# Kernel tuning notes

Measured on AMD Instinct MI355X. Metric: run time of the kernel, lower is better.

Reference implementation:

```python
import jax, jax.numpy as jnp
import numpy as np

B = 1024       # batch of triples
E = 50000      # num_entities
R = 500        # num_relations
D = 512        # dimension
P = 16         # parts
C = 8          # num_cores
ALPHA = 2.0    # -> q = alpha/2 = 1.0
Q = ALPHA / 2.0
DP = D // P    # 32


def setup_inputs() -> dict:
    key = jax.random.key(0)
    ks = jax.random.split(key, 10)
    xav_e = (2.0 / (E + D)) ** 0.5
    xav_r = (2.0 / (R + D)) ** 0.5
    return {
        "heads": jax.random.randint(ks[0], (B,), 0, E),
        "relations": jax.random.randint(ks[1], (B,), 0, R),
        "tails": jax.random.randint(ks[2], (B,), 0, E),
        "entity_w": jax.random.normal(ks[3], (E, D), dtype=jnp.float32) * xav_e,
        "relation_w": jax.random.normal(ks[4], (R, D), dtype=jnp.float32) * xav_r,
        "W_cores": jax.random.uniform(ks[5], (C, P, P, P), dtype=jnp.float32,
                                      minval=-0.01, maxval=0.01),
        "attn_w1": jax.random.normal(ks[6], (2 * D, D), dtype=jnp.float32) * (1.0 / (2 * D)) ** 0.5,
        "attn_b1": jnp.zeros((D,), dtype=jnp.float32),
        "attn_w2": jax.random.normal(ks[7], (D, C), dtype=jnp.float32) * (1.0 / D) ** 0.5,
        "attn_b2": jnp.zeros((C,), dtype=jnp.float32),
    }


def _pq_norm(x):
    # ((|x|^p).sum(2) ** q).sum(1), p=2
    return ((x * x).sum(2) ** Q).sum(1)


def _geometric_consistency(W_cores):
    # center of mass of |W| along each axis, per core; vectorized over cores
    coords = jnp.arange(P, dtype=jnp.float32)
    Wa = jnp.abs(W_cores)                      # [C,P,P,P]
    tot = Wa.sum(axis=(1, 2, 3))               # [C]
    cx = (Wa * coords[None, :, None, None]).sum(axis=(1, 2, 3)) / tot
    cy = (Wa * coords[None, None, :, None]).sum(axis=(1, 2, 3)) / tot
    cz = (Wa * coords[None, None, None, :]).sum(axis=(1, 2, 3)) / tot
    centers = jnp.stack([cx, cy, cz], axis=1)  # [C,3]
    d2 = ((centers[:, None, :] - centers[None, :, :]) ** 2).sum(-1)
    dist = jnp.sqrt(d2)
    masked = dist + jnp.eye(C, dtype=dist.dtype) * 1e6
    min_d = masked.min(axis=1)
    return -jnp.mean(jnp.log(min_d + 1e-6))


def reference(heads, relations, tails, entity_w, relation_w, W_cores,
              attn_w1, attn_b1, attn_w2, attn_b2):
    h = entity_w[heads]          # [B,D]
    r = relation_w[relations]    # [B,D]
    t = entity_w[tails]          # [B,D]

    hr = jnp.concatenate([h, r], axis=1)                       # [B,2D]
    hid = jax.nn.relu(hr @ attn_w1 + attn_b1)                  # [B,D]
    attn = jax.nn.softmax(hid @ attn_w2 + attn_b2, axis=1)     # [B,C]

    h3 = h.reshape(-1, DP, P)
    r3 = r.reshape(-1, DP, P)
    t3 = t.reshape(-1, DP, P)

    h_norm = _pq_norm(h3)
    r_norm = _pq_norm(r3)
    t_norm = _pq_norm(t3)

    # attention-weighted effective core per triple (sum over cores is linear,
    # so folding attn into W before the contraction is exactly the same math)
    Weff = jnp.einsum('bc,cpqs->bpqs', attn, W_cores)          # [B,P,P,P]

    # x1[b,i,s] = sum_{p,q} h[b,i,p] r[b,i,q] W[b,p,q,s]
    x1 = jnp.einsum('bip,biq,bpqs->bis', h3, r3, Weff)
    # x2[b,i,p] = sum_{q,s} r[b,i,q] t[b,i,s] W[b,p,q,s]
    x2 = jnp.einsum('biq,bis,bpqs->bip', r3, t3, Weff)
    # x3[b,i,q] = sum_{p,s} h[b,i,p] t[b,i,s] W[b,p,q,s]
    x3 = jnp.einsum('bip,bis,bpqs->biq', h3, t3, Weff)

    whr_norm = _pq_norm(x1)
    wrt_norm = _pq_norm(x2)
    wth_norm = _pq_norm(x3)

    scores = x1.reshape(-1, D) @ entity_w.T                    # [B,E]

    factor1 = jnp.mean(h_norm) + jnp.mean(r_norm) + jnp.mean(t_norm)
    factor2 = jnp.mean(whr_norm) + jnp.mean(wrt_norm) + jnp.mean(wth_norm)
    factor3 = _geometric_consistency(W_cores)
    return (scores, factor1, factor2, factor3, attn)
```

## Files before the change

### kernel.cpp

```cpp
#include <hip/hip_runtime.h>
#include <cstdint>
#include <cstddef>

#define NB 1024
#define NE 50000
#define NE_PAD 50048
#define DCOL 512
#define ATTN_C 8

static const size_t SCORES_OFF = (size_t)NB * NE;
static const size_t F1_OFF = SCORES_OFF + 0;
static const size_t F2_OFF = SCORES_OFF + 1;
static const size_t F3_OFF = SCORES_OFF + 2;
static const size_t ATTN_OFF = SCORES_OFF + 3;

typedef float f32x4 __attribute__((ext_vector_type(4)));
typedef short s16x8 __attribute__((ext_vector_type(8)));

__device__ __forceinline__ unsigned short f2bf(float f) {
  union { float f; uint32_t u; } x; x.f = f;
  uint32_t u = x.u;
  uint32_t r = (u + 0x7fffu + ((u >> 16) & 1u)) >> 16;
  return (unsigned short)r;
}

__device__ __forceinline__ void gload16(const void* g, void* l) {
  __builtin_amdgcn_global_load_lds(
      (const __attribute__((address_space(1))) uint32_t*)g,
      (__attribute__((address_space(3))) uint32_t*)l, 16, 0, 0);
}

__global__ __launch_bounds__(256)
void gather_hr(const int* __restrict__ heads, const int* __restrict__ rels,
               const int* __restrict__ tails, const float* __restrict__ ew,
               const float* __restrict__ rw, unsigned short* __restrict__ hrb,
               float* __restrict__ n1) {
  int b = blockIdx.x, tid = threadIdx.x;
  const float* h = ew + (size_t)heads[b] * DCOL;
  const float* r = rw + (size_t)rels[b] * DCOL;
  const float* t = ew + (size_t)tails[b] * DCOL;
  float acc = 0.f;
  for (int d = tid; d < DCOL; d += 256) {
    float hv = h[d], rv = r[d], tv = t[d];
    hrb[(size_t)b * 1024 + d] = f2bf(hv);
    hrb[(size_t)b * 1024 + DCOL + d] = f2bf(rv);
    acc += hv * hv + rv * rv + tv * tv;
  }
  __shared__ float red[256];
  red[tid] = acc; __syncthreads();
  for (int s = 128; s > 0; s >>= 1) {
    if (tid < s) red[tid] += red[tid + s];
    __syncthreads();
  }
  if (tid == 0) n1[b] = red[0];
}

__global__ __launch_bounds__(256)
void cvt_pad(const float* __restrict__ src, unsigned short* __restrict__ dst,
             int n4valid, int n4tot) {
  int i = blockIdx.x * 256 + threadIdx.x;
  int stride = gridDim.x * 256;
  for (; i < n4tot; i += stride) {
    float x = 0.f, y = 0.f, z = 0.f, w = 0.f;
    if (i < n4valid) {
      float4 v = ((const float4*)src)[i];
      x = v.x; y = v.y; z = v.z; w = v.w;
    }
    union { unsigned short u[4]; uint2 v2; } o;
    o.u[0] = f2bf(x); o.u[1] = f2bf(y); o.u[2] = f2bf(z); o.u[3] = f2bf(w);
    ((uint2*)dst)[i] = o.v2;
  }
}

__global__ __launch_bounds__(256)
void transpose_w1(const float* __restrict__ w1, unsigned short* __restrict__ w1t) {
  __shared__ float tile[32][33];
  int tx = threadIdx.x & 31, ty = threadIdx.x >> 5;
  int kb = blockIdx.y * 32, nb = blockIdx.x * 32;
  #pragma unroll
  for (int rr = 0; rr < 32; rr += 8)
    tile[ty + rr][tx] = w1[(size_t)(kb + ty + rr) * 512 + nb + tx];
  __syncthreads();
  #pragma unroll
  for (int rr = 0; rr < 32; rr += 8)
    w1t[(size_t)(nb + ty + rr) * 1024 + kb + tx] = f2bf(tile[tx][ty + rr]);
}

template <int EPI>
__global__ __launch_bounds__(256, 2)
void gemm_nt(const unsigned short* __restrict__ A, const unsigned short* __restrict__ B,
             float* __restrict__ C, const float* __restrict__ bias,
             int M, int N, int K, int Nc) {
  __shared__ __align__(16) uint8_t smem[32768];
  const int tid = threadIdx.x;
  const int lane = tid & 63;
  const int wv = tid >> 6;
  const int wm = wv >> 1, wn = wv & 1;
  const int m0 = blockIdx.x * 128;
  const int n0 = blockIdx.y * 128;
  const int rbytes = K * 2;

  f32x4 acc[4][4];
  #pragma unroll
  for (int i = 0; i < 4; ++i)
    #pragma unroll
    for (int j = 0; j < 4; ++j) acc[i][j] = (f32x4){0.f, 0.f, 0.f, 0.f};

  const int srow = lane >> 3;
  const int scol = lane & 7;
  const int nkt = K >> 6;

  for (int kt = 0; kt < nkt; ++kt) {
    #pragma unroll
    for (int j = 0; j < 4; ++j) {
      int chunk = wv * 4 + j;
      int r = chunk * 8 + srow;
      int c = scol ^ (r & 7);
      const uint8_t* ga = (const uint8_t*)A + (size_t)(m0 + r) * rbytes + kt * 128 + c * 16;
      gload16(ga, &smem[chunk * 1024]);
      const uint8_t* gb = (const uint8_t*)B + (size_t)(n0 + r) * rbytes + kt * 128 + c * 16;
      gload16(gb, &smem[16384 + chunk * 1024]);
    }
    __syncthreads();
    #pragma unroll
    for (int kk = 0; kk < 2; ++kk) {
      s16x8 af[4], bfr[4];
      #pragma unroll
      for (int f = 0; f < 4; ++f) {
        int ra = wm * 64 + f * 16 + (lane & 15);
        int ca = (kk * 4 + (lane >> 4)) ^ (ra & 7);
        af[f] = *(const s16x8*)&smem[ra * 128 + ca * 16];
        int rb = wn * 64 + f * 16 + (lane & 15);
        int cb = (kk * 4 + (lane >> 4)) ^ (rb & 7);
        bfr[f] = *(const s16x8*)&smem[16384 + rb * 128 + cb * 16];
      }
      #pragma unroll
      for (int fm = 0; fm < 4; ++fm)
        #pragma unroll
        for (int fn = 0; fn < 4; ++fn)
          acc[fm][fn] = __builtin_amdgcn_mfma_f32_16x16x32_bf16(
              af[fm], bfr[fn], acc[fm][fn], 0, 0, 0);
    }
    __syncthreads();
  }

  const int rl = lane >> 4, cl = lane & 15;
  #pragma unroll
  for (int fm = 0; fm < 4; ++fm)
    #pragma unroll
    for (int fn = 0; fn < 4; ++fn)
      #pragma unroll
      for (int j = 0; j < 4; ++j) {
        int gm = m0 + wm * 64 + fm * 16 + rl * 4 + j;
        int gn = n0 + wn * 64 + fn * 16 + cl;
        if (gn < Nc) {
          float v = acc[fm][fn][j];
          if (EPI) v = fmaxf(v + bias[gn], 0.f);
          C[(size_t)gm * Nc + gn] = v;
        }
      }
}

__global__ __launch_bounds__(256)
void attn_softmax(const float* __restrict__ hid, const float* __restrict__ w2,
                  const float* __restrict__ b2, float* __restrict__ attn_out) {
  int b = blockIdx.x, tid = threadIdx.x;
  float acc[8] = {0, 0, 0, 0, 0, 0, 0, 0};
  for (int k = tid; k < DCOL; k += 256) {
    float hv = hid[(size_t)b * DCOL + k];
    #pragma unroll
    for (int c = 0; c < 8; ++c) acc[c] += hv * w2[k * 8 + c];
  }
  __shared__ float red[256];
  __shared__ float logits[8];
  for (int c = 0; c < 8; ++c) {
    red[tid] = acc[c]; __syncthreads();
    for (int s = 128; s > 0; s >>= 1) {
      if (tid < s) red[tid] += red[tid + s];
      __syncthreads();
    }
    if (tid == 0) logits[c] = red[0] + b2[c];
    __syncthreads();
  }
  if (tid == 0) {
    float mx = logits[0];
    #pragma unroll
    for (int c = 1; c < 8; ++c) mx = fmaxf(mx, logits[c]);
    float e[8]; float s = 0.f;
    #pragma unroll
    for (int c = 0; c < 8; ++c) { e[c] = expf(logits[c] - mx); s += e[c]; }
    #pragma unroll
    for (int c = 0; c < 8; ++c) attn_out[(size_t)b * 8 + c] = e[c] / s;
  }
}

__global__ __launch_bounds__(256, 2)
void triple_core(const int* __restrict__ heads, const int* __restrict__ rels,
                 const int* __restrict__ tails, const float* __restrict__ ew,
                 const float* __restrict__ rw, const float* __restrict__ wc,
                 const float* __restrict__ attn, unsigned short* __restrict__ x1b,
                 float* __restrict__ n2) {
  __shared__ float hs[512], rs[512], ts[512];
  __shared__ __align__(16) float W123[4096][4];
  __shared__ float att[8];
  __shared__ float red[256];
  int b = blockIdx.x, tid = threadIdx.x;
  const float* hp_ = ew + (size_t)heads[b] * DCOL;
  const float* rp_ = rw + (size_t)rels[b] * DCOL;
  const float* tp_ = ew + (size_t)tails[b] * DCOL;
  #pragma unroll
  for (int it = 0; it < 2; ++it) {
    int d = it * 256 + tid;
    hs[d] = hp_[d]; rs[d] = rp_[d]; ts[d] = tp_[d];
  }
  if (tid < 8) att[tid] = attn[(size_t)b * 8 + tid];
  __syncthreads();
  #pragma unroll
  for (int it = 0; it < 16; ++it) {
    int idx = it * 256 + tid;
    float w = 0.f;
    #pragma unroll
    for (int c = 0; c < 8; ++c) w = fmaf(att[c], wc[c * 4096 + idx], w);
    int s = idx & 15, q = (idx >> 4) & 15, p = idx >> 8;
    W123[idx][0] = w;
    W123[(q * 16 + s) * 16 + p][1] = w;
    W123[(p * 16 + s) * 16 + q][2] = w;
  }
  __syncthreads();

  const int so = tid & 15;
  const int i0 = tid >> 4, i1 = i0 + 16;
  float h0[16], r0[16], t0[16], h1[16], r1[16], t1[16];
  #pragma unroll
  for (int k = 0; k < 16; ++k) {
    h0[k] = hs[i0 * 16 + k]; r0[k] = rs[i0 * 16 + k]; t0[k] = ts[i0 * 16 + k];
    h1[k] = hs[i1 * 16 + k]; r1[k] = rs[i1 * 16 + k]; t1[k] = ts[i1 * 16 + k];
  }
  float a10 = 0.f, a20 = 0.f, a30 = 0.f, a11 = 0.f, a21 = 0.f, a31 = 0.f;
  const float4* wp = (const float4*)&W123[so][0];
  #pragma unroll
  for (int u = 0; u < 16; ++u) {
    #pragma unroll
    for (int v = 0; v < 16; ++v) {
      float4 w = wp[u * 256 + v * 16];
      a10 = fmaf(h0[u] * r0[v], w.x, a10);
      a20 = fmaf(r0[u] * t0[v], w.y, a20);
      a30 = fmaf(h0[u] * t0[v], w.z, a30);
      a11 = fmaf(h1[u] * r1[v], w.x, a11);
      a21 = fmaf(r1[u] * t1[v], w.y, a21);
      a31 = fmaf(h1[u] * t1[v], w.z, a31);
    }
  }
  x1b[(size_t)b * 512 + i0 * 16 + so] = f2bf(a10);
  x1b[(size_t)b * 512 + i1 * 16 + so] = f2bf(a11);
  red[tid] = a10 * a10 + a20 * a20 + a30 * a30
           + a11 * a11 + a21 * a21 + a31 * a31;
  __syncthreads();
  for (int s = 128; s > 0; s >>= 1) {
    if (tid < s) red[tid] += red[tid + s];
    __syncthreads();
  }
  if (tid == 0) n2[b] = red[0];
}

__global__ __launch_bounds__(256)
void finalize(const float* __restrict__ n1, const float* __restrict__ n2,
              const float* __restrict__ wc, float* __restrict__ out) {
  int tid = threadIdx.x;
  __shared__ float red[256];
  float a = 0.f;
  for (int i = tid; i < NB; i += 256) a += n1[i];
  red[tid] = a; __syncthreads();
  for (int s = 128; s > 0; s >>= 1) { if (tid < s) red[tid] += red[tid + s]; __syncthreads(); }
  if (tid == 0) out[F1_OFF] = red[0] / (float)NB;
  __syncthreads();
  a = 0.f;
  for (int i = tid; i < NB; i += 256) a += n2[i];
  red[tid] = a; __syncthreads();
  for (int s = 128; s > 0; s >>= 1) { if (tid < s) red[tid] += red[tid + s]; __syncthreads(); }
  if (tid == 0) out[F2_OFF] = red[0] / (float)NB;
  __syncthreads();

  int c = tid >> 5, l = tid & 31;
  float tot = 0.f, cx = 0.f, cy = 0.f, cz = 0.f;
  for (int e = l; e < 4096; e += 32) {
    float w = fabsf(wc[c * 4096 + e]);
    int z = e & 15, y = (e >> 4) & 15, x = e >> 8;
    tot += w; cx += w * x; cy += w * y; cz += w * z;
  }
  #pragma unroll
  for (int off = 16; off > 0; off >>= 1) {
    tot += __shfl_down(tot, off);
    cx += __shfl_down(cx, off);
    cy += __shfl_down(cy, off);
    cz += __shfl_down(cz, off);
  }
  __shared__ float cent[8][3];
  if (l == 0) { cent[c][0] = cx / tot; cent[c][1] = cy / tot; cent[c][2] = cz / tot; }
  __syncthreads();
  if (tid == 0) {
    float f3 = 0.f;
    for (int i = 0; i < 8; ++i) {
      float mn = 1e30f;
      for (int j = 0; j < 8; ++j) {
        if (j == i) continue;
        float dx = cent[i][0] - cent[j][0];
        float dy = cent[i][1] - cent[j][1];
        float dz = cent[i][2] - cent[j][2];
        float d = sqrtf(dx * dx + dy * dy + dz * dz);
        mn = fminf(mn, d);
      }
      f3 += logf(mn + 1e-6f);
    }
    out[F3_OFF] = -f3 / 8.f;
  }
}

extern "C" void kernel_launch(void* const* d_in, const int* in_sizes, int n_in,
                              void* d_out, int out_size, void* d_ws, size_t ws_size,
                              hipStream_t stream) {
  const int* heads = (const int*)d_in[0];
  const int* rels = (const int*)d_in[1];
  const int* tails = (const int*)d_in[2];
  const float* ew = (const float*)d_in[3];
  const float* rw = (const float*)d_in[4];
  const float* wc = (const float*)d_in[5];
  const float* w1 = (const float*)d_in[6];
  const float* b1 = (const float*)d_in[7];
  const float* w2 = (const float*)d_in[8];
  const float* b2 = (const float*)d_in[9];
  float* out = (float*)d_out;

  uint8_t* ws = (uint8_t*)d_ws;
  const size_t EWB_SZ = (size_t)NE_PAD * DCOL * 2;
  unsigned short* ewb = (unsigned short*)ws;
  unsigned short* hrb = (unsigned short*)(ws + EWB_SZ);
  unsigned short* w1t = (unsigned short*)(ws + EWB_SZ + 2097152);
  float* hid = (float*)(ws + EWB_SZ + 2097152 + 1048576);
  unsigned short* x1b = (unsigned short*)(ws + EWB_SZ + 2097152 + 1048576 + 2097152);
  float* n1 = (float*)(ws + EWB_SZ + 2097152 + 1048576 + 2097152 + 1048576);
  float* n2 = n1 + NB;

  gather_hr<<<NB, 256, 0, stream>>>(heads, rels, tails, ew, rw, hrb, n1);
  cvt_pad<<<2048, 256, 0, stream>>>(ew, ewb, NE * DCOL / 4, NE_PAD * DCOL / 4);
  transpose_w1<<<dim3(16, 32), 256, 0, stream>>>(w1, w1t);
  gemm_nt<1><<<dim3(8, 4), 256, 0, stream>>>(hrb, w1t, hid, b1, 1024, 512, 1024, 512);
  attn_softmax<<<NB, 256, 0, stream>>>(hid, w2, b2, out + ATTN_OFF);
  triple_core<<<NB, 256, 0, stream>>>(heads, rels, tails, ew, rw, wc,
                                      out + ATTN_OFF, x1b, n2);
  gemm_nt<0><<<dim3(8, NE_PAD / 128), 256, 0, stream>>>(x1b, ewb, out, nullptr,
                                                        1024, NE_PAD, 512, NE);
  finalize<<<1, 256, 0, stream>>>(n1, n2, wc, out);
}
```

Before: 253.2 us.

## Fuse fp32-to-bf16 entity conversion into score GEMM and merge small kernels

```diff
diff --git a/kernel.cpp b/kernel.cpp
--- a/kernel.cpp
+++ b/kernel.cpp
@@ -4,7 +4,6 @@
 
 #define NB 1024
 #define NE 50000
-#define NE_PAD 50048
 #define DCOL 512
 #define ATTN_C 8
 
@@ -31,80 +30,71 @@
 }
 
 __global__ __launch_bounds__(256)
-void gather_hr(const int* __restrict__ heads, const int* __restrict__ rels,
-               const int* __restrict__ tails, const float* __restrict__ ew,
-               const float* __restrict__ rw, unsigned short* __restrict__ hrb,
-               float* __restrict__ n1) {
-  int b = blockIdx.x, tid = threadIdx.x;
-  const float* h = ew + (size_t)heads[b] * DCOL;
-  const float* r = rw + (size_t)rels[b] * DCOL;
-  const float* t = ew + (size_t)tails[b] * DCOL;
-  float acc = 0.f;
-  for (int d = tid; d < DCOL; d += 256) {
-    float hv = h[d], rv = r[d], tv = t[d];
-    hrb[(size_t)b * 1024 + d] = f2bf(hv);
-    hrb[(size_t)b * 1024 + DCOL + d] = f2bf(rv);
-    acc += hv * hv + rv * rv + tv * tv;
-  }
-  __shared__ float red[256];
-  red[tid] = acc; __syncthreads();
-  for (int s = 128; s > 0; s >>= 1) {
-    if (tid < s) red[tid] += red[tid + s];
+void prep(const int* __restrict__ heads, const int* __restrict__ rels,
+          const int* __restrict__ tails, const float* __restrict__ ew,
+          const float* __restrict__ rw, const float* __restrict__ w1,
+          unsigned short* __restrict__ hrb, unsigned short* __restrict__ w1t,
+          float* __restrict__ n1) {
+  int tid = threadIdx.x;
+  if (blockIdx.x < NB) {
+    int b = blockIdx.x;
+    const float* h = ew + (size_t)heads[b] * DCOL;
+    const float* r = rw + (size_t)rels[b] * DCOL;
+    const float* t = ew + (size_t)tails[b] * DCOL;
+    float acc = 0.f;
+    #pragma unroll
+    for (int it = 0; it < 2; ++it) {
+      int d = it * 256 + tid;
+      float hv = h[d], rv = r[d], tv = t[d];
+      hrb[(size_t)b * 1024 + d] = f2bf(hv);
+      hrb[(size_t)b * 1024 + DCOL + d] = f2bf(rv);
+      acc += hv * hv + rv * rv + tv * tv;
+    }
+    __shared__ float red[256];
+    red[tid] = acc; __syncthreads();
+    for (int s = 128; s > 0; s >>= 1) {
+      if (tid < s) red[tid] += red[tid + s];
+      __syncthreads();
+    }
+    if (tid == 0) n1[b] = red[0];
+  } else {
+    int tb = blockIdx.x - NB;
+    int nb = (tb & 15) * 32, kb = (tb >> 4) * 32;
+    __shared__ float tile[32][33];
+    int tx = tid & 31, ty = tid >> 5;
+    #pragma unroll
+    for (int rr = 0; rr < 32; rr += 8)
+      tile[ty + rr][tx] = w1[(size_t)(kb + ty + rr) * 512 + nb + tx];
     __syncthreads();
-  }
-  if (tid == 0) n1[b] = red[0];
-}
-
-__global__ __launch_bounds__(256)
-void cvt_pad(const float* __restrict__ src, unsigned short* __restrict__ dst,
-             int n4valid, int n4tot) {
-  int i = blockIdx.x * 256 + threadIdx.x;
-  int stride = gridDim.x * 256;
-  for (; i < n4tot; i += stride) {
-    float x = 0.f, y = 0.f, z = 0.f, w = 0.f;
-    if (i < n4valid) {
-      float4 v = ((const float4*)src)[i];
-      x = v.x; y = v.y; z = v.z; w = v.w;
-    }
-    union { unsigned short u[4]; uint2 v2; } o;
-    o.u[0] = f2bf(x); o.u[1] = f2bf(y); o.u[2] = f2bf(z); o.u[3] = f2bf(w);
-    ((uint2*)dst)[i] = o.v2;
-  }
-}
-
-__global__ __launch_bounds__(256)
-void transpose_w1(const float* __restrict__ w1, unsigned short* __restrict__ w1t) {
-  __shared__ float tile[32][33];
-  int tx = threadIdx.x & 31, ty = threadIdx.x >> 5;
-  int kb = blockIdx.y * 32, nb = blockIdx.x * 32;
-  #pragma unroll
-  for (int rr = 0; rr < 32; rr += 8)
-    tile[ty + rr][tx] = w1[(size_t)(kb + ty + rr) * 512 + nb + tx];
-  __syncthreads();
-  #pragma unroll
-  for (int rr = 0; rr < 32; rr += 8)
-    w1t[(size_t)(nb + ty + rr) * 1024 + kb + tx] = f2bf(tile[tx][ty + rr]);
-}
-
-template <int EPI>
+    #pragma unroll
+    for (int rr = 0; rr < 32; rr += 8)
+      w1t[(size_t)(nb + ty + rr) * 1024 + kb + tx] = f2bf(tile[tx][ty + rr]);
+  }
+}
+
+template <int EPI, int FR, int BF32>
 __global__ __launch_bounds__(256, 2)
-void gemm_nt(const unsigned short* __restrict__ A, const unsigned short* __restrict__ B,
+void gemm_nt(const unsigned short* __restrict__ A,
+             const unsigned short* __restrict__ Bb,
+             const float* __restrict__ Bf,
              float* __restrict__ C, const float* __restrict__ bias,
-             int M, int N, int K, int Nc) {
-  __shared__ __align__(16) uint8_t smem[32768];
+             int M, int N, int K, int Nc, int NrowsB) {
+  constexpr int BM = FR * 32;
+  constexpr int SMEM_A = BM * 128;
+  __shared__ __align__(16) uint8_t smem[2 * SMEM_A];
   const int tid = threadIdx.x;
   const int lane = tid & 63;
   const int wv = tid >> 6;
   const int wm = wv >> 1, wn = wv & 1;
-  const int m0 = blockIdx.x * 128;
-  const int n0 = blockIdx.y * 128;
+  const int m0 = blockIdx.x * BM;
+  const int n0 = blockIdx.y * BM;
   const int rbytes = K * 2;
 
-  f32x4 acc[4][4];
-  #pragma unroll
-  for (int i = 0; i < 4; ++i)
-    #pragma unroll
-    for (int j = 0; j < 4; ++j) acc[i][j] = (f32x4){0.f, 0.f, 0.f, 0.f};
+  f32x4 acc[FR][FR];
+  #pragma unroll
+  for (int i = 0; i < FR; ++i)
+    #pragma unroll
+    for (int j = 0; j < FR; ++j) acc[i][j] = (f32x4){0.f, 0.f, 0.f, 0.f};
 
   const int srow = lane >> 3;
   const int scol = lane & 7;
@@ -112,32 +102,45 @@
 
   for (int kt = 0; kt < nkt; ++kt) {
     #pragma unroll
-    for (int j = 0; j < 4; ++j) {
-      int chunk = wv * 4 + j;
+    for (int j = 0; j < FR; ++j) {
+      int chunk = wv * FR + j;
       int r = chunk * 8 + srow;
       int c = scol ^ (r & 7);
       const uint8_t* ga = (const uint8_t*)A + (size_t)(m0 + r) * rbytes + kt * 128 + c * 16;
       gload16(ga, &smem[chunk * 1024]);
-      const uint8_t* gb = (const uint8_t*)B + (size_t)(n0 + r) * rbytes + kt * 128 + c * 16;
-      gload16(gb, &smem[16384 + chunk * 1024]);
+      if (BF32) {
+        int rn = n0 + r; rn = rn < NrowsB ? rn : NrowsB - 1;
+        const float* src = Bf + (size_t)rn * K + kt * 64 + c * 8;
+        float4 v0 = *(const float4*)src;
+        float4 v1 = *(const float4*)(src + 4);
+        s16x8 o;
+        o[0] = (short)f2bf(v0.x); o[1] = (short)f2bf(v0.y);
+        o[2] = (short)f2bf(v0.z); o[3] = (short)f2bf(v0.w);
+        o[4] = (short)f2bf(v1.x); o[5] = (short)f2bf(v1.y);
+        o[6] = (short)f2bf(v1.z); o[7] = (short)f2bf(v1.w);
+        *(s16x8*)&smem[SMEM_A + chunk * 1024 + srow * 128 + scol * 16] = o;
+      } else {
+        const uint8_t* gb = (const uint8_t*)Bb + (size_t)(n0 + r) * rbytes + kt * 128 + c * 16;
+        gload16(gb, &smem[SMEM_A + chunk * 1024]);
+      }
     }
     __syncthreads();
     #pragma unroll
     for (int kk = 0; kk < 2; ++kk) {
-      s16x8 af[4], bfr[4];
+      s16x8 af[FR], bfr[FR];
       #pragma unroll
-      for (int f = 0; f < 4; ++f) {
-        int ra = wm * 64 + f * 16 + (lane & 15);
+      for (int f = 0; f < FR; ++f) {
+        int ra = wm * 16 * FR + f * 16 + (lane & 15);
         int ca = (kk * 4 + (lane >> 4)) ^ (ra & 7);
         af[f] = *(const s16x8*)&smem[ra * 128 + ca * 16];
-        int rb = wn * 64 + f * 16 + (lane & 15);
+        int rb = wn * 16 * FR + f * 16 + (lane & 15);
         int cb = (kk * 4 + (lane >> 4)) ^ (rb & 7);
-        bfr[f] = *(const s16x8*)&smem[16384 + rb * 128 + cb * 16];
+        bfr[f] = *(const s16x8*)&smem[SMEM_A + rb * 128 + cb * 16];
       }
       #pragma unroll
-      for (int fm = 0; fm < 4; ++fm)
+      for (int fm = 0; fm < FR; ++fm)
         #pragma unroll
-        for (int fn = 0; fn < 4; ++fn)
+        for (int fn = 0; fn < FR; ++fn)
           acc[fm][fn] = __builtin_amdgcn_mfma_f32_16x16x32_bf16(
               af[fm], bfr[fn], acc[fm][fn], 0, 0, 0);
     }
@@ -146,13 +149,13 @@
 
   const int rl = lane >> 4, cl = lane & 15;
   #pragma unroll
-  for (int fm = 0; fm < 4; ++fm)
-    #pragma unroll
-    for (int fn = 0; fn < 4; ++fn)
+  for (int fm = 0; fm < FR; ++fm)
+    #pragma unroll
+    for (int fn = 0; fn < FR; ++fn)
       #pragma unroll
       for (int j = 0; j < 4; ++j) {
-        int gm = m0 + wm * 64 + fm * 16 + rl * 4 + j;
-        int gn = n0 + wn * 64 + fn * 16 + cl;
+        int gm = m0 + wm * 16 * FR + fm * 16 + rl * 4 + j;
+        int gn = n0 + wn * 16 * FR + fn * 16 + cl;
         if (gn < Nc) {
           float v = acc[fm][fn][j];
           if (EPI) v = fmaxf(v + bias[gn], 0.f);
@@ -161,59 +164,58 @@
       }
 }
 
-__global__ __launch_bounds__(256)
-void attn_softmax(const float* __restrict__ hid, const float* __restrict__ w2,
-                  const float* __restrict__ b2, float* __restrict__ attn_out) {
-  int b = blockIdx.x, tid = threadIdx.x;
-  float acc[8] = {0, 0, 0, 0, 0, 0, 0, 0};
-  for (int k = tid; k < DCOL; k += 256) {
-    float hv = hid[(size_t)b * DCOL + k];
-    #pragma unroll
-    for (int c = 0; c < 8; ++c) acc[c] += hv * w2[k * 8 + c];
-  }
-  __shared__ float red[256];
-  __shared__ float logits[8];
-  for (int c = 0; c < 8; ++c) {
-    red[tid] = acc[c]; __syncthreads();
-    for (int s = 128; s > 0; s >>= 1) {
-      if (tid < s) red[tid] += red[tid + s];
-      __syncthreads();
-    }
-    if (tid == 0) logits[c] = red[0] + b2[c];
-    __syncthreads();
-  }
-  if (tid == 0) {
-    float mx = logits[0];
-    #pragma unroll
-    for (int c = 1; c < 8; ++c) mx = fmaxf(mx, logits[c]);
-    float e[8]; float s = 0.f;
-    #pragma unroll
-    for (int c = 0; c < 8; ++c) { e[c] = expf(logits[c] - mx); s += e[c]; }
-    #pragma unroll
-    for (int c = 0; c < 8; ++c) attn_out[(size_t)b * 8 + c] = e[c] / s;
-  }
-}
-
 __global__ __launch_bounds__(256, 2)
 void triple_core(const int* __restrict__ heads, const int* __restrict__ rels,
                  const int* __restrict__ tails, const float* __restrict__ ew,
                  const float* __restrict__ rw, const float* __restrict__ wc,
-                 const float* __restrict__ attn, unsigned short* __restrict__ x1b,
-                 float* __restrict__ n2) {
+                 const float* __restrict__ hid, const float* __restrict__ w2,
+                 const float* __restrict__ b2, float* __restrict__ attn_out,
+                 unsigned short* __restrict__ x1b, float* __restrict__ n2) {
   __shared__ float hs[512], rs[512], ts[512];
   __shared__ __align__(16) float W123[4096][4];
   __shared__ float att[8];
+  __shared__ float wred[4][8];
   __shared__ float red[256];
   int b = blockIdx.x, tid = threadIdx.x;
+  int lane = tid & 63, wid = tid >> 6;
   const float* hp_ = ew + (size_t)heads[b] * DCOL;
   const float* rp_ = rw + (size_t)rels[b] * DCOL;
   const float* tp_ = ew + (size_t)tails[b] * DCOL;
+  float la[8] = {0, 0, 0, 0, 0, 0, 0, 0};
   #pragma unroll
   for (int it = 0; it < 2; ++it) {
     int d = it * 256 + tid;
     hs[d] = hp_[d]; rs[d] = rp_[d]; ts[d] = tp_[d];
-  }
-  if (tid < 8) att[tid] = attn[(size_t)b * 8 + tid];
+    float hv = hid[(size_t)b * DCOL + d];
+    #pragma unroll
+    for (int c = 0; c < 8; ++c) la[c] = fmaf(hv, w2[d * 8 + c], la[c]);
+  }
+  #pragma unroll
+  for (int off = 32; off > 0; off >>= 1)
+    #pragma unroll
+    for (int c = 0; c < 8; ++c) la[c] += __shfl_down(la[c], off);
+  if (lane == 0)
+    #pragma unroll
+    for (int c = 0; c < 8; ++c) wred[wid][c] = la[c];
+  __syncthreads();
+  if (tid == 0) {
+    float lg[8];
+    #pragma unroll
+    for (int c = 0; c < 8; ++c)
+      lg[c] = wred[0][c] + wred[1][c] + wred[2][c] + wred[3][c] + b2[c];
+    float mx = lg[0];
+    #pragma unroll
+    for (int c = 1; c < 8; ++c) mx = fmaxf(mx, lg[c]);
+    float e[8], s = 0.f;
+    #pragma unroll
+    for (int c = 0; c < 8; ++c) { e[c] = expf(lg[c] - mx); s += e[c]; }
+    #pragma unroll
+    for (int c = 0; c < 8; ++c) {
+      float a = e[c] / s;
+      att[c] = a;
+      attn_out[(size_t)b * 8 + c] = a;
+    }
+  }
   __syncthreads();
   #pragma unroll
   for (int it = 0; it < 16; ++it) {
@@ -332,23 +334,19 @@
   float* out = (float*)d_out;
 
   uint8_t* ws = (uint8_t*)d_ws;
-  const size_t EWB_SZ = (size_t)NE_PAD * DCOL * 2;
-  unsigned short* ewb = (unsigned short*)ws;
-  unsigned short* hrb = (unsigned short*)(ws + EWB_SZ);
-  unsigned short* w1t = (unsigned short*)(ws + EWB_SZ + 2097152);
-  float* hid = (float*)(ws + EWB_SZ + 2097152 + 1048576);
-  unsigned short* x1b = (unsigned short*)(ws + EWB_SZ + 2097152 + 1048576 + 2097152);
-  float* n1 = (float*)(ws + EWB_SZ + 2097152 + 1048576 + 2097152 + 1048576);
+  unsigned short* hrb = (unsigned short*)ws;
+  unsigned short* w1t = (unsigned short*)(ws + 2097152);
+  float* hid = (float*)(ws + 2097152 + 1048576);
+  unsigned short* x1b = (unsigned short*)(ws + 2097152 + 1048576 + 2097152);
+  float* n1 = (float*)(ws + 2097152 + 1048576 + 2097152 + 1048576);
   float* n2 = n1 + NB;
 
-  gather_hr<<<NB, 256, 0, stream>>>(heads, rels, tails, ew, rw, hrb, n1);
-  cvt_pad<<<2048, 256, 0, stream>>>(ew, ewb, NE * DCOL / 4, NE_PAD * DCOL / 4);
-  transpose_w1<<<dim3(16, 32), 256, 0, stream>>>(w1, w1t);
-  gemm_nt<1><<<dim3(8, 4), 256, 0, stream>>>(hrb, w1t, hid, b1, 1024, 512, 1024, 512);
-  attn_softmax<<<NB, 256, 0, stream>>>(hid, w2, b2, out + ATTN_OFF);
+  prep<<<NB + 512, 256, 0, stream>>>(heads, rels, tails, ew, rw, w1, hrb, w1t, n1);
+  gemm_nt<1, 2, 0><<<dim3(16, 8), 256, 0, stream>>>(
+      hrb, w1t, nullptr, hid, b1, 1024, 512, 1024, 512, 512);
   triple_core<<<NB, 256, 0, stream>>>(heads, rels, tails, ew, rw, wc,
-                                      out + ATTN_OFF, x1b, n2);
-  gemm_nt<0><<<dim3(8, NE_PAD / 128), 256, 0, stream>>>(x1b, ewb, out, nullptr,
-                                                        1024, NE_PAD, 512, NE);
+                                      hid, w2, b2, out + ATTN_OFF, x1b, n2);
+  gemm_nt<0, 4, 1><<<dim3(8, 391), 256, 0, stream>>>(
+      x1b, nullptr, ew, out, nullptr, 1024, 50048, 512, NE, NE);
   finalize<<<1, 256, 0, stream>>>(n1, n2, wc, out);
 }
```

Result: no change. 254.6 us (+0.5%).
